# Performance work log

Hardware: AMD Instinct MI355X
Metric: run time of the kernel (lower is better)

The kernel has to match this reference:

```python
import jax, jax.numpy as jnp
import numpy as np

PROX_THRESH = 50.0
NEG_SLOPE = 0.2  # PyG GATConv default leaky_relu slope


def _layer_norm(x, g, b, eps=1e-5):
    m = x.mean(-1, keepdims=True)
    v = x.var(-1, keepdims=True)
    return (x - m) / jnp.sqrt(v + eps) * g + b


def _forward(ego_agent_past, neighbor_agents_past, node_w, node_b, node_ln_g,
             node_ln_b, ego_w, ego_b, ego_ln_g, ego_ln_b, gat_w, gat_asrc,
             gat_adst, gat_b, proj_w, proj_b):
    B = ego_agent_past.shape[0]
    ego_last = ego_agent_past[:, -1, :5]            # [B,5]
    nbr_last = neighbor_agents_past[:, :, -1, :5]   # [B,Nn,5]
    x = jnp.concatenate([ego_last[:, None], nbr_last], axis=1)  # [B,N,5]
    N = x.shape[1]
    dim = node_w.shape[1]
    heads, C = gat_asrc.shape[1], gat_asrc.shape[2]

    # build_graph: edge (j->i) iff dist(i,j) < 50 and i != j; GATConv then
    # adds self-loops, so the diagonal is always connected.
    pos = x[..., :2]
    d2 = jnp.sum((pos[:, :, None, :] - pos[:, None, :, :]) ** 2, axis=-1)  # [B,N,N]
    eye = jnp.eye(N, dtype=bool)
    adj = ((jnp.sqrt(d2) < PROX_THRESH) & ~eye) | eye   # adj[b,i,j]: msg j -> i

    # node features zero-padded from 5 -> 11 columns (as in forward)
    nf = jnp.pad(x, ((0, 0), (0, 0), (0, 11 - x.shape[-1])))
    h_node = _layer_norm(jax.nn.relu(nf @ node_w + node_b), node_ln_g, node_ln_b)
    h_ego = _layer_norm(jax.nn.relu(nf[..., :7] @ ego_w + ego_b), ego_ln_g, ego_ln_b)
    is_ego = (jnp.arange(N) == 0)  # node 0 of every scene is the ego
    h = jnp.where(is_ego[None, :, None], h_ego, h_node)  # [B,N,dim]

    # GATConv layers (eval mode, dropout inactive), concat=True
    for l in range(gat_w.shape[0]):
        wh = (h @ gat_w[l]).reshape(B, N, heads, C)                    # [B,N,H,C]
        a_s = jnp.einsum('bnhc,hc->bnh', wh, gat_asrc[l])              # source term
        a_d = jnp.einsum('bnhc,hc->bnh', wh, gat_adst[l])              # dest term
        # e[b,i,j,h] for edge j->i
        e = jax.nn.leaky_relu(a_s[:, None, :, :] + a_d[:, :, None, :], NEG_SLOPE)
        e = jnp.where(adj[..., None], e, -1e9)
        alpha = jax.nn.softmax(e, axis=2)                              # over sources j
        out = jnp.einsum('bijh,bjhc->bihc', alpha, wh).reshape(B, N, dim) + gat_b[l]
        h = jax.nn.relu(out)

    h = h @ proj_w + proj_b
    # all agents are valid (randn features have nonzero abs-sum), so no padding
    mask = jnp.zeros((B, N), dtype=bool)
    return h, mask


def setup_inputs() -> dict:
    key = jax.random.key(0)
    ks = jax.random.split(key, 10)
    B, Nn, T = 16, 1023, 20
    dim, heads, L = 256, 4, 2
    C = dim // heads
    f = lambda i, s: jax.random.normal(ks[i], s, dtype=jnp.float32)
    return {
        'ego_agent_past': f(0, (B, T, 7)),
        'neighbor_agents_past': f(1, (B, Nn, T, 11)),
        'node_w': f(2, (11, dim)) * 0.1, 'node_b': jnp.zeros((dim,), jnp.float32),
        'node_ln_g': jnp.ones((dim,), jnp.float32), 'node_ln_b': jnp.zeros((dim,), jnp.float32),
        'ego_w': f(3, (7, dim)) * 0.1, 'ego_b': jnp.zeros((dim,), jnp.float32),
        'ego_ln_g': jnp.ones((dim,), jnp.float32), 'ego_ln_b': jnp.zeros((dim,), jnp.float32),
        'gat_w': f(4, (L, dim, dim)) * 0.1,
        'gat_asrc': f(5, (L, heads, C)) * 0.1,
        'gat_adst': f(6, (L, heads, C)) * 0.1,
        'gat_b': jnp.zeros((L, dim), jnp.float32),
        'proj_w': f(7, (dim, dim)) * 0.1, 'proj_b': jnp.zeros((dim,), jnp.float32),
    }


def reference(ego_agent_past, neighbor_agents_past, node_w, node_b, node_ln_g,
              node_ln_b, ego_w, ego_b, ego_ln_g, ego_ln_b, gat_w, gat_asrc,
              gat_adst, gat_b, proj_w, proj_b):
    return _forward(ego_agent_past, neighbor_agents_past, node_w, node_b,
                    node_ln_g, node_ln_b, ego_w, ego_b, ego_ln_g, ego_ln_b,
                    gat_w, gat_asrc, gat_adst, gat_b, proj_w, proj_b)
```

## Files before the change

kernel.cpp:

```cpp
#include <hip/hip_runtime.h>
#include <cstddef>

typedef _Float16 f16;
typedef _Float16 f16x8 __attribute__((ext_vector_type(8)));
typedef _Float16 f16x4 __attribute__((ext_vector_type(4)));
typedef float f32x4 __attribute__((ext_vector_type(4)));

#define BATCH 16
#define NAGENT 1024
#define NNBR 1023
#define TSTEP 20
#define DIM 256
#define ROWS 16384
#define TH2 2500.0f
#define LOG2E 1.44269504089f

#define O_PX   0
#define O_PY   16384
#define O_H16  32768
#define O_AS   2129920
#define O_AD   2195456
#define O_M    2260992
#define O_US   2261056
#define O_UD   2263104
#define O_WT   2265152
#define O_ADJ  2363456

__global__ __launch_bounds__(256) void node_embed(
    const float* __restrict__ ego, const float* __restrict__ nbr,
    const float* __restrict__ node_w, const float* __restrict__ node_b,
    const float* __restrict__ node_g, const float* __restrict__ node_beta,
    const float* __restrict__ ego_w, const float* __restrict__ ego_b,
    const float* __restrict__ ego_g, const float* __restrict__ ego_beta,
    f16* __restrict__ h16, float* __restrict__ px, float* __restrict__ py) {
    int w = threadIdx.x >> 6, lane = threadIdx.x & 63;
    int row = blockIdx.x * 4 + w;
    int b = row >> 10, n = row & 1023;
    const float* src;
    if (n == 0) src = ego + (size_t)b * TSTEP * 7 + (TSTEP - 1) * 7;
    else        src = nbr + (((size_t)b * NNBR + (n - 1)) * TSTEP + (TSTEP - 1)) * 11;
    const float *W, *bias, *g, *beta;
    if (n == 0) { W = ego_w;  bias = ego_b;  g = ego_g;  beta = ego_beta; }
    else        { W = node_w; bias = node_b; g = node_g; beta = node_beta; }
    float xv[5];
#pragma unroll
    for (int k = 0; k < 5; k++) xv[k] = src[k];
    if (lane == 0) { px[row] = xv[0]; py[row] = xv[1]; }
    int c0 = lane * 4;
    float4 bv = *(const float4*)(bias + c0);
    float acc[4] = {bv.x, bv.y, bv.z, bv.w};
#pragma unroll
    for (int k = 0; k < 5; k++) {
        float4 wv = *(const float4*)(W + (size_t)k * 256 + c0);
        acc[0] = fmaf(xv[k], wv.x, acc[0]);
        acc[1] = fmaf(xv[k], wv.y, acc[1]);
        acc[2] = fmaf(xv[k], wv.z, acc[2]);
        acc[3] = fmaf(xv[k], wv.w, acc[3]);
    }
#pragma unroll
    for (int c = 0; c < 4; c++) acc[c] = fmaxf(acc[c], 0.f);
    float s1 = acc[0] + acc[1] + acc[2] + acc[3];
    float s2 = acc[0]*acc[0] + acc[1]*acc[1] + acc[2]*acc[2] + acc[3]*acc[3];
#pragma unroll
    for (int off = 1; off < 64; off <<= 1) {
        s1 += __shfl_xor(s1, off);
        s2 += __shfl_xor(s2, off);
    }
    float mean = s1 * (1.f / 256.f);
    float var  = s2 * (1.f / 256.f) - mean * mean;
    float rstd = rsqrtf(var + 1e-5f);
    float4 gv = *(const float4*)(g + c0);
    float4 be = *(const float4*)(beta + c0);
    f16x4 o;
    o[0] = (f16)((acc[0] - mean) * rstd * gv.x + be.x);
    o[1] = (f16)((acc[1] - mean) * rstd * gv.y + be.y);
    o[2] = (f16)((acc[2] - mean) * rstd * gv.z + be.z);
    o[3] = (f16)((acc[3] - mean) * rstd * gv.w + be.w);
    *(f16x4*)(h16 + (size_t)row * 256 + c0) = o;
}

__global__ __launch_bounds__(256) void adj_build(const float* __restrict__ px,
                                                 const float* __restrict__ py,
                                                 unsigned char* __restrict__ mask) {
    int blk = blockIdx.x;
    int b = blk >> 6, ic = blk & 63;
    int base = b << 10;
    __shared__ float sx[1024], sy[1024];
    int t = threadIdx.x;
#pragma unroll
    for (int i = 0; i < 4; i++) {
        sx[t + i * 256] = px[base + t + i * 256];
        sy[t + i * 256] = py[base + t + i * 256];
    }
    __syncthreads();
    int i_loc = t >> 4;
    int s = (t >> 3) & 1;
    int q = (t >> 1) & 3;
    int chalf = t & 1;
    int ig = ic * 16 + i_loc;
    float xi = sx[ig], yi = sy[ig];
    unsigned int w0 = 0, w1 = 0;
#pragma unroll
    for (int cc = 0; cc < 8; cc++) {
        int c = chalf * 8 + cc;
        unsigned int byte = 0;
        int j0 = s * 512 + c * 32 + q * 8;
#pragma unroll
        for (int jj = 0; jj < 8; jj++) {
            int j = j0 + jj;
            float dx = sx[j] - xi, dy = sy[j] - yi;
            if ((dx * dx + dy * dy < TH2) || (j == ig)) byte |= 1u << jj;
        }
        if (cc < 4) w0 |= byte << (cc * 8);
        else        w1 |= byte << ((cc - 4) * 8);
    }
    uint2 v; v.x = w0; v.y = w1;
    *(uint2*)(mask + (((size_t)(base + ig)) << 7) + s * 64 + q * 16 + chalf * 8) = v;
}

__global__ __launch_bounds__(256) void prep_weights(
    const float* __restrict__ gat_w, const float* __restrict__ proj_w,
    const float* __restrict__ asrc, const float* __restrict__ adst,
    f16* __restrict__ WT, float* __restrict__ us, float* __restrict__ ud) {
    int bid = blockIdx.x;
    int t = threadIdx.x;
    if (bid < 48) {
        int m = bid >> 4, t4 = bid & 15;
        int ti = (t4 >> 2) * 64;
        int tj = (t4 & 3) * 64;
        const float* W = (m < 2) ? (gat_w + (size_t)m * 65536) : proj_w;
        __shared__ float ls[64][68];
#pragma unroll
        for (int i = 0; i < 4; i++) {
            int idx = t + i * 256;
            int r = idx >> 4, c4 = (idx & 15) * 4;
            float4 v = *(const float4*)(W + (size_t)(ti + r) * 256 + tj + c4);
            ls[r][c4] = v.x; ls[r][c4 + 1] = v.y; ls[r][c4 + 2] = v.z; ls[r][c4 + 3] = v.w;
        }
        __syncthreads();
#pragma unroll
        for (int i = 0; i < 2; i++) {
            int idx = t + i * 256;
            int nr = idx >> 3, kc = (idx & 7) * 8;
            f16x8 v;
#pragma unroll
            for (int j = 0; j < 8; j++) v[j] = (f16)ls[kc + j][nr];
            *(f16x8*)(WT + (size_t)m * 65536 + (size_t)(tj + nr) * 256 + ti + kc) = v;
        }
    } else {
        int blk = bid - 48;
        int l = blk >> 2, h = blk & 3;
        const float* W  = gat_w + (size_t)l * 65536 + t * 256 + h * 64;
        const float* as = asrc + l * 256 + h * 64;
        const float* ad = adst + l * 256 + h * 64;
        float s = 0.f, d = 0.f;
#pragma unroll 8
        for (int c = 0; c < 64; c++) { s = fmaf(W[c], as[c], s); d = fmaf(W[c], ad[c], d); }
        us[blk * 256 + t] = s;
        ud[blk * 256 + t] = d;
    }
}

__global__ __launch_bounds__(256, 4) void gemm_f16(
    const f16* __restrict__ A, const f16* __restrict__ BT,
    f16* __restrict__ whT, float* __restrict__ outF, const float* __restrict__ bias,
    const float* __restrict__ us, const float* __restrict__ ud,
    float* __restrict__ a_sT, float* __restrict__ a_dT) {
    __shared__ f16 sA[32 * 264];
    __shared__ float sU[8 * 256];
    int t = threadIdx.x;
    int m0 = blockIdx.x * 32;
    {
        int r = t >> 3, u0 = (t & 7) * 4;
        const f16* gp = A + (size_t)(m0 + r) * 256 + u0 * 8;
        f16* lp = sA + r * 264 + u0 * 8;
#pragma unroll
        for (int u = 0; u < 4; u++)
            *(f16x8*)(lp + u * 8) = *(const f16x8*)(gp + u * 8);
    }
    if (us) {
#pragma unroll
        for (int i = 0; i < 4; i++) sU[t + i * 256] = us[t + i * 256];
#pragma unroll
        for (int i = 0; i < 4; i++) sU[1024 + t + i * 256] = ud[t + i * 256];
    }
    __syncthreads();
    int w = t >> 6, lane = t & 63, il = lane & 15, q = lane >> 4;
    int n0 = w * 64;
    f32x4 acc[2][4];
#pragma unroll
    for (int mt = 0; mt < 2; mt++)
#pragma unroll
        for (int nt = 0; nt < 4; nt++) acc[mt][nt] = (f32x4){0.f, 0.f, 0.f, 0.f};
    const f16* Bp  = BT + (size_t)(n0 + il) * 256 + q * 8;
    const f16* Ap0 = sA + il * 264 + q * 8;
#pragma unroll 2
    for (int ks = 0; ks < 256; ks += 32) {
        f16x8 a0 = *(const f16x8*)(Ap0 + ks);
        f16x8 a1 = *(const f16x8*)(Ap0 + 16 * 264 + ks);
        f16x8 b0 = *(const f16x8*)(Bp + ks);
        f16x8 b1 = *(const f16x8*)(Bp + 16 * 256 + ks);
        f16x8 b2 = *(const f16x8*)(Bp + 32 * 256 + ks);
        f16x8 b3 = *(const f16x8*)(Bp + 48 * 256 + ks);
        acc[0][0] = __builtin_amdgcn_mfma_f32_16x16x32_f16(a0, b0, acc[0][0], 0, 0, 0);
        acc[0][1] = __builtin_amdgcn_mfma_f32_16x16x32_f16(a0, b1, acc[0][1], 0, 0, 0);
        acc[0][2] = __builtin_amdgcn_mfma_f32_16x16x32_f16(a0, b2, acc[0][2], 0, 0, 0);
        acc[0][3] = __builtin_amdgcn_mfma_f32_16x16x32_f16(a0, b3, acc[0][3], 0, 0, 0);
        acc[1][0] = __builtin_amdgcn_mfma_f32_16x16x32_f16(a1, b0, acc[1][0], 0, 0, 0);
        acc[1][1] = __builtin_amdgcn_mfma_f32_16x16x32_f16(a1, b1, acc[1][1], 0, 0, 0);
        acc[1][2] = __builtin_amdgcn_mfma_f32_16x16x32_f16(a1, b2, acc[1][2], 0, 0, 0);
        acc[1][3] = __builtin_amdgcn_mfma_f32_16x16x32_f16(a1, b3, acc[1][3], 0, 0, 0);
    }
    if (whT) {
#pragma unroll
        for (int mt = 0; mt < 2; mt++)
#pragma unroll
            for (int nt = 0; nt < 4; nt++) {
                f16x4 v;
#pragma unroll
                for (int reg = 0; reg < 4; reg++) v[reg] = (f16)acc[mt][nt][reg];
                *(f16x4*)(whT + (size_t)(n0 + nt * 16 + il) * ROWS + m0 + mt * 16 + q * 4) = v;
            }
    } else {
#pragma unroll
        for (int nt = 0; nt < 4; nt++) {
            float bv = bias[n0 + nt * 16 + il];
#pragma unroll
            for (int mt = 0; mt < 2; mt++)
#pragma unroll
                for (int reg = 0; reg < 4; reg++)
                    outF[(size_t)(m0 + mt * 16 + q * 4 + reg) * 256 + n0 + nt * 16 + il] =
                        acc[mt][nt][reg] + bv;
        }
    }
    if (us) {
        int r2 = t >> 3, sub = t & 7;
        int hh = sub & 3, isD = sub >> 2;
        const float* uv = sU + isD * 1024 + hh * 256;
        const f16* ar = sA + r2 * 264;
        float d0 = 0.f;
#pragma unroll 4
        for (int kk = 0; kk < 32; kk++) {
            f16x8 av = *(const f16x8*)(ar + kk * 8);
            float4 u0 = *(const float4*)(uv + kk * 8);
            float4 u1 = *(const float4*)(uv + kk * 8 + 4);
            d0 += (float)av[0] * u0.x + (float)av[1] * u0.y +
                  (float)av[2] * u0.z + (float)av[3] * u0.w +
                  (float)av[4] * u1.x + (float)av[5] * u1.y +
                  (float)av[6] * u1.z + (float)av[7] * u1.w;
        }
        float* dst = isD ? a_dT : a_sT;
        dst[(size_t)hh * ROWS + m0 + r2] = d0;
    }
}

__global__ __launch_bounds__(256) void reduce_max(const float* __restrict__ a_sT,
                                                  float* __restrict__ M) {
    int blk = blockIdx.x;
    int b = blk >> 2, h = blk & 3;
    const float* p = a_sT + (size_t)h * ROWS + b * NAGENT;
    int t = threadIdx.x;
    float m = fmaxf(fmaxf(p[t], p[t + 256]), fmaxf(p[t + 512], p[t + 768]));
#pragma unroll
    for (int off = 32; off > 0; off >>= 1) m = fmaxf(m, __shfl_down(m, off));
    __shared__ float red[4];
    if ((t & 63) == 0) red[t >> 6] = m;
    __syncthreads();
    if (t == 0) M[blk] = fmaxf(fmaxf(red[0], red[1]), fmaxf(red[2], red[3]));
}

__global__ __launch_bounds__(512, 4) void gat_attn(
    const f16* __restrict__ whT, const float* __restrict__ a_sT,
    const float* __restrict__ a_dT, const unsigned char* __restrict__ mask,
    const float* __restrict__ M, const float* __restrict__ gat_b,
    f16* __restrict__ h16out) {
    __shared__ f32x4 comb[4][64][10];
    int t = threadIdx.x;
    int w = t >> 6, lane = t & 63;
    int h = w & 3, s = w >> 2;
    int blk = blockIdx.x;
    int b = blk >> 5;
    int i0 = (blk & 31) << 5;
    int base = b << 10;
    int il = lane & 15, q = lane >> 4;
    int ig0 = i0 + il, ig1 = i0 + 16 + il;

    float Mh = M[b * 4 + h];
    float adv0 = a_dT[(size_t)h * ROWS + base + ig0];
    float adv1 = a_dT[(size_t)h * ROWS + base + ig1];
    float mz0 = Mh + adv0, mz1 = Mh + adv1;
    float mi0 = fmaxf(mz0, 0.2f * mz0), mi1 = fmaxf(mz1, 0.2f * mz1);
    float nm0 = -mi0 * LOG2E, nm1 = -mi1 * LOG2E;

    uint4 mq0 = *(const uint4*)(mask + (((size_t)(base + ig0)) << 7) + s * 64 + q * 16);
    uint4 mq1 = *(const uint4*)(mask + (((size_t)(base + ig1)) << 7) + s * 64 + q * 16);
    unsigned int mw0[4] = {mq0.x, mq0.y, mq0.z, mq0.w};
    unsigned int mw1[4] = {mq1.x, mq1.y, mq1.z, mq1.w};

    f32x4 acc[2][5];
#pragma unroll
    for (int mt = 0; mt < 2; mt++)
#pragma unroll
        for (int nt = 0; nt < 5; nt++) acc[mt][nt] = (f32x4){0.f, 0.f, 0.f, 0.f};
    f16x8 ones;
#pragma unroll
    for (int j = 0; j < 8; j++) ones[j] = (f16)1.f;

    int jbase = base + (s << 9);
    const f16*   wp  = whT + (size_t)(h * 64 + il) * ROWS + jbase + q * 8;
    const float* asp = a_sT + (size_t)h * ROWS + jbase + q * 8;

    for (int c = 0; c < 16; ++c) {
        int j0 = c * 32;
        f16x8 b0 = *(const f16x8*)(wp + j0);
        f16x8 b1 = *(const f16x8*)(wp + (size_t)16 * ROWS + j0);
        f16x8 b2 = *(const f16x8*)(wp + (size_t)32 * ROWS + j0);
        f16x8 b3 = *(const f16x8*)(wp + (size_t)48 * ROWS + j0);
        float4 as0 = *(const float4*)(asp + j0);
        float4 as1 = *(const float4*)(asp + j0 + 4);
        unsigned int mb0 = (mw0[c >> 2] >> ((c & 3) * 8)) & 255u;
        unsigned int mb1 = (mw1[c >> 2] >> ((c & 3) * 8)) & 255u;
        float asv[8] = {as0.x, as0.y, as0.z, as0.w, as1.x, as1.y, as1.z, as1.w};
        f16x8 afr0, afr1;
#pragma unroll
        for (int jj = 0; jj < 8; ++jj) {
            float z = asv[jj];
            float z0 = z + adv0, z1 = z + adv1;
            float sc0 = fmaxf(z0, 0.2f * z0), sc1 = fmaxf(z1, 0.2f * z1);
            float e0 = exp2f(fmaf(sc0, LOG2E, nm0));
            float e1 = exp2f(fmaf(sc1, LOG2E, nm1));
            afr0[jj] = (f16)(((mb0 >> jj) & 1u) ? e0 : 0.f);
            afr1[jj] = (f16)(((mb1 >> jj) & 1u) ? e1 : 0.f);
        }
        acc[0][0] = __builtin_amdgcn_mfma_f32_16x16x32_f16(afr0, b0, acc[0][0], 0, 0, 0);
        acc[1][0] = __builtin_amdgcn_mfma_f32_16x16x32_f16(afr1, b0, acc[1][0], 0, 0, 0);
        acc[0][1] = __builtin_amdgcn_mfma_f32_16x16x32_f16(afr0, b1, acc[0][1], 0, 0, 0);
        acc[1][1] = __builtin_amdgcn_mfma_f32_16x16x32_f16(afr1, b1, acc[1][1], 0, 0, 0);
        acc[0][2] = __builtin_amdgcn_mfma_f32_16x16x32_f16(afr0, b2, acc[0][2], 0, 0, 0);
        acc[1][2] = __builtin_amdgcn_mfma_f32_16x16x32_f16(afr1, b2, acc[1][2], 0, 0, 0);
        acc[0][3] = __builtin_amdgcn_mfma_f32_16x16x32_f16(afr0, b3, acc[0][3], 0, 0, 0);
        acc[1][3] = __builtin_amdgcn_mfma_f32_16x16x32_f16(afr1, b3, acc[1][3], 0, 0, 0);
        acc[0][4] = __builtin_amdgcn_mfma_f32_16x16x32_f16(afr0, ones, acc[0][4], 0, 0, 0);
        acc[1][4] = __builtin_amdgcn_mfma_f32_16x16x32_f16(afr1, ones, acc[1][4], 0, 0, 0);
    }
    if (s == 1) {
#pragma unroll
        for (int mt = 0; mt < 2; mt++)
#pragma unroll
            for (int nt = 0; nt < 5; nt++) comb[h][lane][mt * 5 + nt] = acc[mt][nt];
    }
    __syncthreads();
    if (s == 0) {
#pragma unroll
        for (int mt = 0; mt < 2; mt++)
#pragma unroll
            for (int nt = 0; nt < 5; nt++) acc[mt][nt] += comb[h][lane][mt * 5 + nt];
        float b0v = gat_b[h * 64 + il];
        float b1v = gat_b[h * 64 + 16 + il];
        float b2v = gat_b[h * 64 + 32 + il];
        float b3v = gat_b[h * 64 + 48 + il];
#pragma unroll
        for (int mt = 0; mt < 2; mt++) {
#pragma unroll
            for (int reg = 0; reg < 4; ++reg) {
                float inv = 1.f / acc[mt][4][reg];
                size_t ro = (size_t)(base + i0 + mt * 16 + q * 4 + reg) * DIM + h * 64 + il;
                h16out[ro +  0] = (f16)fmaxf(fmaf(acc[mt][0][reg], inv, b0v), 0.f);
                h16out[ro + 16] = (f16)fmaxf(fmaf(acc[mt][1][reg], inv, b1v), 0.f);
                h16out[ro + 32] = (f16)fmaxf(fmaf(acc[mt][2][reg], inv, b2v), 0.f);
                h16out[ro + 48] = (f16)fmaxf(fmaf(acc[mt][3][reg], inv, b3v), 0.f);
            }
        }
    }
}

__global__ void zero_mask(float* __restrict__ p) {
    p[blockIdx.x * 256 + threadIdx.x] = 0.f;
}

extern "C" void kernel_launch(void* const* d_in, const int* in_sizes, int n_in,
                              void* d_out, int out_size, void* d_ws, size_t ws_size,
                              hipStream_t stream) {
    const float* ego       = (const float*)d_in[0];
    const float* nbr       = (const float*)d_in[1];
    const float* node_w    = (const float*)d_in[2];
    const float* node_b    = (const float*)d_in[3];
    const float* node_g    = (const float*)d_in[4];
    const float* node_beta = (const float*)d_in[5];
    const float* ego_w     = (const float*)d_in[6];
    const float* ego_b     = (const float*)d_in[7];
    const float* ego_g     = (const float*)d_in[8];
    const float* ego_beta  = (const float*)d_in[9];
    const float* gat_w     = (const float*)d_in[10];
    const float* gat_asrc  = (const float*)d_in[11];
    const float* gat_adst  = (const float*)d_in[12];
    const float* gat_bias  = (const float*)d_in[13];
    const float* proj_w    = (const float*)d_in[14];
    const float* proj_b    = (const float*)d_in[15];

    float* out = (float*)d_out;
    float* ws  = (float*)d_ws;
    float* px   = ws + O_PX;
    float* py   = ws + O_PY;
    f16*   h16  = (f16*)(ws + O_H16);
    float* asT  = ws + O_AS;
    float* adT  = ws + O_AD;
    float* Mmax = ws + O_M;
    float* us   = ws + O_US;
    float* ud   = ws + O_UD;
    f16*   WT   = (f16*)(ws + O_WT);
    unsigned char* adj = (unsigned char*)(ws + O_ADJ);
    f16*   whT  = (f16*)d_out;

    node_embed<<<4096, 256, 0, stream>>>(ego, nbr, node_w, node_b, node_g, node_beta,
                                         ego_w, ego_b, ego_g, ego_beta, h16, px, py);
    adj_build<<<1024, 256, 0, stream>>>(px, py, adj);
    prep_weights<<<56, 256, 0, stream>>>(gat_w, proj_w, gat_asrc, gat_adst, WT, us, ud);
    for (int l = 0; l < 2; l++) {
        gemm_f16<<<512, 256, 0, stream>>>(h16, WT + (size_t)l * 65536, whT, nullptr, nullptr,
                                          us + l * 1024, ud + l * 1024, asT, adT);
        reduce_max<<<64, 256, 0, stream>>>(asT, Mmax);
        gat_attn<<<512, 512, 0, stream>>>(whT, asT, adT, adj, Mmax,
                                          gat_bias + l * 256, h16);
    }
    gemm_f16<<<512, 256, 0, stream>>>(h16, WT + (size_t)2 * 65536, nullptr, out, proj_b,
                                      nullptr, nullptr, nullptr, nullptr);
    zero_mask<<<64, 256, 0, stream>>>(out + (size_t)ROWS * DIM);
}
```

Before: 252.4 us.

## Fuse prep kernels into one launch and fold source-max into GEMM via atomics

Merges node embedding, adjacency build, weight transpose, tail zeroing and Mmax init into a single mega_prep launch. The adjacency blocks now read positions straight from the inputs instead of an intermediate px/py buffer. The separate reduce_max kernel is removed: each GEMM block reduces its 32 a_s values per head and applies a CAS-based atomic max. The change also transposes the comb shared-memory layout in gat_attn and unrolls its main loop by two. The aim is fewer launches and less inter-kernel traffic, at the cost of atomic contention, an extra __syncthreads in the GEMM epilogue, and a heterogeneous grid.

Measured after the change: 259.9 us. +3.0%, slower.

```diff
diff --git a/kernel.cpp b/kernel.cpp
--- a/kernel.cpp
+++ b/kernel.cpp
@@ -14,150 +14,165 @@
 #define ROWS 16384
 #define TH2 2500.0f
 #define LOG2E 1.44269504089f
-
-#define O_PX   0
-#define O_PY   16384
-#define O_H16  32768
-#define O_AS   2129920
-#define O_AD   2195456
-#define O_M    2260992
-#define O_US   2261056
-#define O_UD   2263104
-#define O_WT   2265152
-#define O_ADJ  2363456
-
-__global__ __launch_bounds__(256) void node_embed(
+#define NEGBIG -3.0e38f
+
+#define O_H16  0
+#define O_AS   2097152
+#define O_AD   2162688
+#define O_US   2228224
+#define O_UD   2230272
+#define O_WT   2232320
+#define O_ADJ  2330624
+#define O_M    2854912
+
+__device__ inline void atomicMaxF(float* addr, float val) {
+    int* ai = (int*)addr;
+    int old = __float_as_int(*addr);
+    while (__int_as_float(old) < val) {
+        int assumed = old;
+        old = atomicCAS(ai, assumed, __float_as_int(val));
+        if (old == assumed) break;
+    }
+}
+
+__global__ __launch_bounds__(256) void mega_prep(
     const float* __restrict__ ego, const float* __restrict__ nbr,
     const float* __restrict__ node_w, const float* __restrict__ node_b,
     const float* __restrict__ node_g, const float* __restrict__ node_beta,
     const float* __restrict__ ego_w, const float* __restrict__ ego_b,
     const float* __restrict__ ego_g, const float* __restrict__ ego_beta,
-    f16* __restrict__ h16, float* __restrict__ px, float* __restrict__ py) {
-    int w = threadIdx.x >> 6, lane = threadIdx.x & 63;
-    int row = blockIdx.x * 4 + w;
-    int b = row >> 10, n = row & 1023;
-    const float* src;
-    if (n == 0) src = ego + (size_t)b * TSTEP * 7 + (TSTEP - 1) * 7;
-    else        src = nbr + (((size_t)b * NNBR + (n - 1)) * TSTEP + (TSTEP - 1)) * 11;
-    const float *W, *bias, *g, *beta;
-    if (n == 0) { W = ego_w;  bias = ego_b;  g = ego_g;  beta = ego_beta; }
-    else        { W = node_w; bias = node_b; g = node_g; beta = node_beta; }
-    float xv[5];
-#pragma unroll
-    for (int k = 0; k < 5; k++) xv[k] = src[k];
-    if (lane == 0) { px[row] = xv[0]; py[row] = xv[1]; }
-    int c0 = lane * 4;
-    float4 bv = *(const float4*)(bias + c0);
-    float acc[4] = {bv.x, bv.y, bv.z, bv.w};
-#pragma unroll
-    for (int k = 0; k < 5; k++) {
-        float4 wv = *(const float4*)(W + (size_t)k * 256 + c0);
-        acc[0] = fmaf(xv[k], wv.x, acc[0]);
-        acc[1] = fmaf(xv[k], wv.y, acc[1]);
-        acc[2] = fmaf(xv[k], wv.z, acc[2]);
-        acc[3] = fmaf(xv[k], wv.w, acc[3]);
-    }
-#pragma unroll
-    for (int c = 0; c < 4; c++) acc[c] = fmaxf(acc[c], 0.f);
-    float s1 = acc[0] + acc[1] + acc[2] + acc[3];
-    float s2 = acc[0]*acc[0] + acc[1]*acc[1] + acc[2]*acc[2] + acc[3]*acc[3];
-#pragma unroll
-    for (int off = 1; off < 64; off <<= 1) {
-        s1 += __shfl_xor(s1, off);
-        s2 += __shfl_xor(s2, off);
-    }
-    float mean = s1 * (1.f / 256.f);
-    float var  = s2 * (1.f / 256.f) - mean * mean;
-    float rstd = rsqrtf(var + 1e-5f);
-    float4 gv = *(const float4*)(g + c0);
-    float4 be = *(const float4*)(beta + c0);
-    f16x4 o;
-    o[0] = (f16)((acc[0] - mean) * rstd * gv.x + be.x);
-    o[1] = (f16)((acc[1] - mean) * rstd * gv.y + be.y);
-    o[2] = (f16)((acc[2] - mean) * rstd * gv.z + be.z);
-    o[3] = (f16)((acc[3] - mean) * rstd * gv.w + be.w);
-    *(f16x4*)(h16 + (size_t)row * 256 + c0) = o;
-}
-
-__global__ __launch_bounds__(256) void adj_build(const float* __restrict__ px,
-                                                 const float* __restrict__ py,
-                                                 unsigned char* __restrict__ mask) {
-    int blk = blockIdx.x;
-    int b = blk >> 6, ic = blk & 63;
-    int base = b << 10;
-    __shared__ float sx[1024], sy[1024];
-    int t = threadIdx.x;
-#pragma unroll
-    for (int i = 0; i < 4; i++) {
-        sx[t + i * 256] = px[base + t + i * 256];
-        sy[t + i * 256] = py[base + t + i * 256];
-    }
-    __syncthreads();
-    int i_loc = t >> 4;
-    int s = (t >> 3) & 1;
-    int q = (t >> 1) & 3;
-    int chalf = t & 1;
-    int ig = ic * 16 + i_loc;
-    float xi = sx[ig], yi = sy[ig];
-    unsigned int w0 = 0, w1 = 0;
-#pragma unroll
-    for (int cc = 0; cc < 8; cc++) {
-        int c = chalf * 8 + cc;
-        unsigned int byte = 0;
-        int j0 = s * 512 + c * 32 + q * 8;
-#pragma unroll
-        for (int jj = 0; jj < 8; jj++) {
-            int j = j0 + jj;
-            float dx = sx[j] - xi, dy = sy[j] - yi;
-            if ((dx * dx + dy * dy < TH2) || (j == ig)) byte |= 1u << jj;
-        }
-        if (cc < 4) w0 |= byte << (cc * 8);
-        else        w1 |= byte << ((cc - 4) * 8);
-    }
-    uint2 v; v.x = w0; v.y = w1;
-    *(uint2*)(mask + (((size_t)(base + ig)) << 7) + s * 64 + q * 16 + chalf * 8) = v;
-}
-
-__global__ __launch_bounds__(256) void prep_weights(
     const float* __restrict__ gat_w, const float* __restrict__ proj_w,
     const float* __restrict__ asrc, const float* __restrict__ adst,
-    f16* __restrict__ WT, float* __restrict__ us, float* __restrict__ ud) {
+    f16* __restrict__ h16, unsigned char* __restrict__ mask,
+    f16* __restrict__ WT, float* __restrict__ us, float* __restrict__ ud,
+    float* __restrict__ Mmax, float* __restrict__ outTail) {
+    __shared__ float smem[64 * 68];
     int bid = blockIdx.x;
     int t = threadIdx.x;
-    if (bid < 48) {
-        int m = bid >> 4, t4 = bid & 15;
-        int ti = (t4 >> 2) * 64;
-        int tj = (t4 & 3) * 64;
-        const float* W = (m < 2) ? (gat_w + (size_t)m * 65536) : proj_w;
-        __shared__ float ls[64][68];
+    if (bid < 4096) {
+        int w = t >> 6, lane = t & 63;
+        int row = bid * 4 + w;
+        int b = row >> 10, n = row & 1023;
+        const float* src;
+        if (n == 0) src = ego + (size_t)b * TSTEP * 7 + (TSTEP - 1) * 7;
+        else        src = nbr + (((size_t)b * NNBR + (n - 1)) * TSTEP + (TSTEP - 1)) * 11;
+        const float *W, *bias, *g, *beta;
+        if (n == 0) { W = ego_w;  bias = ego_b;  g = ego_g;  beta = ego_beta; }
+        else        { W = node_w; bias = node_b; g = node_g; beta = node_beta; }
+        float xv[5];
+#pragma unroll
+        for (int k = 0; k < 5; k++) xv[k] = src[k];
+        int c0 = lane * 4;
+        float4 bv = *(const float4*)(bias + c0);
+        float acc[4] = {bv.x, bv.y, bv.z, bv.w};
+#pragma unroll
+        for (int k = 0; k < 5; k++) {
+            float4 wv = *(const float4*)(W + (size_t)k * 256 + c0);
+            acc[0] = fmaf(xv[k], wv.x, acc[0]);
+            acc[1] = fmaf(xv[k], wv.y, acc[1]);
+            acc[2] = fmaf(xv[k], wv.z, acc[2]);
+            acc[3] = fmaf(xv[k], wv.w, acc[3]);
+        }
+#pragma unroll
+        for (int c = 0; c < 4; c++) acc[c] = fmaxf(acc[c], 0.f);
+        float s1 = acc[0] + acc[1] + acc[2] + acc[3];
+        float s2 = acc[0]*acc[0] + acc[1]*acc[1] + acc[2]*acc[2] + acc[3]*acc[3];
+#pragma unroll
+        for (int off = 1; off < 64; off <<= 1) {
+            s1 += __shfl_xor(s1, off);
+            s2 += __shfl_xor(s2, off);
+        }
+        float mean = s1 * (1.f / 256.f);
+        float var  = s2 * (1.f / 256.f) - mean * mean;
+        float rstd = rsqrtf(var + 1e-5f);
+        float4 gv = *(const float4*)(g + c0);
+        float4 be = *(const float4*)(beta + c0);
+        f16x4 o;
+        o[0] = (f16)((acc[0] - mean) * rstd * gv.x + be.x);
+        o[1] = (f16)((acc[1] - mean) * rstd * gv.y + be.y);
+        o[2] = (f16)((acc[2] - mean) * rstd * gv.z + be.z);
+        o[3] = (f16)((acc[3] - mean) * rstd * gv.w + be.w);
+        *(f16x4*)(h16 + (size_t)row * 256 + c0) = o;
+    } else if (bid < 5120) {
+        int bid2 = bid - 4096;
+        int b = bid2 >> 6, ic = bid2 & 63;
+        int base = b << 10;
+        float* sx = smem;
+        float* sy = smem + 1024;
 #pragma unroll
         for (int i = 0; i < 4; i++) {
-            int idx = t + i * 256;
-            int r = idx >> 4, c4 = (idx & 15) * 4;
-            float4 v = *(const float4*)(W + (size_t)(ti + r) * 256 + tj + c4);
-            ls[r][c4] = v.x; ls[r][c4 + 1] = v.y; ls[r][c4 + 2] = v.z; ls[r][c4 + 3] = v.w;
+            int r = t + i * 256;
+            const float* srcp = (r == 0)
+                ? (ego + (size_t)b * TSTEP * 7 + (TSTEP - 1) * 7)
+                : (nbr + (((size_t)b * NNBR + (r - 1)) * TSTEP + (TSTEP - 1)) * 11);
+            sx[r] = srcp[0];
+            sy[r] = srcp[1];
         }
         __syncthreads();
-#pragma unroll
-        for (int i = 0; i < 2; i++) {
-            int idx = t + i * 256;
-            int nr = idx >> 3, kc = (idx & 7) * 8;
-            f16x8 v;
-#pragma unroll
-            for (int j = 0; j < 8; j++) v[j] = (f16)ls[kc + j][nr];
-            *(f16x8*)(WT + (size_t)m * 65536 + (size_t)(tj + nr) * 256 + ti + kc) = v;
-        }
+        int i_loc = t >> 4;
+        int s = (t >> 3) & 1;
+        int q = (t >> 1) & 3;
+        int chalf = t & 1;
+        int ig = ic * 16 + i_loc;
+        float xi = sx[ig], yi = sy[ig];
+        unsigned int w0 = 0, w1 = 0;
+#pragma unroll
+        for (int cc = 0; cc < 8; cc++) {
+            int c = chalf * 8 + cc;
+            unsigned int byte = 0;
+            int j0 = s * 512 + c * 32 + q * 8;
+#pragma unroll
+            for (int jj = 0; jj < 8; jj++) {
+                int j = j0 + jj;
+                float dx = sx[j] - xi, dy = sy[j] - yi;
+                if ((dx * dx + dy * dy < TH2) || (j == ig)) byte |= 1u << jj;
+            }
+            if (cc < 4) w0 |= byte << (cc * 8);
+            else        w1 |= byte << ((cc - 4) * 8);
+        }
+        uint2 v; v.x = w0; v.y = w1;
+        *(uint2*)(mask + (((size_t)(base + ig)) << 7) + s * 64 + q * 16 + chalf * 8) = v;
+    } else if (bid < 5176) {
+        int bid3 = bid - 5120;
+        if (bid3 < 48) {
+            int m = bid3 >> 4, t4 = bid3 & 15;
+            int ti = (t4 >> 2) * 64;
+            int tj = (t4 & 3) * 64;
+            const float* W = (m < 2) ? (gat_w + (size_t)m * 65536) : proj_w;
+            float (*ls)[68] = (float(*)[68])smem;
+#pragma unroll
+            for (int i = 0; i < 4; i++) {
+                int idx = t + i * 256;
+                int r = idx >> 4, c4 = (idx & 15) * 4;
+                float4 v = *(const float4*)(W + (size_t)(ti + r) * 256 + tj + c4);
+                ls[r][c4] = v.x; ls[r][c4 + 1] = v.y; ls[r][c4 + 2] = v.z; ls[r][c4 + 3] = v.w;
+            }
+            __syncthreads();
+#pragma unroll
+            for (int i = 0; i < 2; i++) {
+                int idx = t + i * 256;
+                int nr = idx >> 3, kc = (idx & 7) * 8;
+                f16x8 v;
+#pragma unroll
+                for (int j = 0; j < 8; j++) v[j] = (f16)ls[kc + j][nr];
+                *(f16x8*)(WT + (size_t)m * 65536 + (size_t)(tj + nr) * 256 + ti + kc) = v;
+            }
+        } else {
+            int blk = bid3 - 48;
+            int l = blk >> 2, h = blk & 3;
+            const float* W  = gat_w + (size_t)l * 65536 + t * 256 + h * 64;
+            const float* as = asrc + l * 256 + h * 64;
+            const float* ad = adst + l * 256 + h * 64;
+            float s = 0.f, d = 0.f;
+#pragma unroll 8
+            for (int c = 0; c < 64; c++) { s = fmaf(W[c], as[c], s); d = fmaf(W[c], ad[c], d); }
+            us[blk * 256 + t] = s;
+            ud[blk * 256 + t] = d;
+        }
+    } else if (bid < 5240) {
+        outTail[(bid - 5176) * 256 + t] = 0.f;
     } else {
-        int blk = bid - 48;
-        int l = blk >> 2, h = blk & 3;
-        const float* W  = gat_w + (size_t)l * 65536 + t * 256 + h * 64;
-        const float* as = asrc + l * 256 + h * 64;
-        const float* ad = adst + l * 256 + h * 64;
-        float s = 0.f, d = 0.f;
-#pragma unroll 8
-        for (int c = 0; c < 64; c++) { s = fmaf(W[c], as[c], s); d = fmaf(W[c], ad[c], d); }
-        us[blk * 256 + t] = s;
-        ud[blk * 256 + t] = d;
+        if (t < 128) Mmax[t] = NEGBIG;
     }
 }
 
@@ -165,9 +180,10 @@
     const f16* __restrict__ A, const f16* __restrict__ BT,
     f16* __restrict__ whT, float* __restrict__ outF, const float* __restrict__ bias,
     const float* __restrict__ us, const float* __restrict__ ud,
-    float* __restrict__ a_sT, float* __restrict__ a_dT) {
+    float* __restrict__ a_sT, float* __restrict__ a_dT, float* __restrict__ Mmax) {
     __shared__ f16 sA[32 * 264];
     __shared__ float sU[8 * 256];
+    __shared__ float redmax[4][32];
     int t = threadIdx.x;
     int m0 = blockIdx.x * 32;
     {
@@ -251,22 +267,15 @@
         }
         float* dst = isD ? a_dT : a_sT;
         dst[(size_t)hh * ROWS + m0 + r2] = d0;
-    }
-}
-
-__global__ __launch_bounds__(256) void reduce_max(const float* __restrict__ a_sT,
-                                                  float* __restrict__ M) {
-    int blk = blockIdx.x;
-    int b = blk >> 2, h = blk & 3;
-    const float* p = a_sT + (size_t)h * ROWS + b * NAGENT;
-    int t = threadIdx.x;
-    float m = fmaxf(fmaxf(p[t], p[t + 256]), fmaxf(p[t + 512], p[t + 768]));
-#pragma unroll
-    for (int off = 32; off > 0; off >>= 1) m = fmaxf(m, __shfl_down(m, off));
-    __shared__ float red[4];
-    if ((t & 63) == 0) red[t >> 6] = m;
-    __syncthreads();
-    if (t == 0) M[blk] = fmaxf(fmaxf(red[0], red[1]), fmaxf(red[2], red[3]));
+        if (!isD) redmax[hh][r2] = d0;
+        __syncthreads();
+        if (t < 4) {
+            float m = redmax[t][0];
+#pragma unroll
+            for (int k = 1; k < 32; k++) m = fmaxf(m, redmax[t][k]);
+            atomicMaxF(&Mmax[(m0 >> 10) * 4 + t], m);
+        }
+    }
 }
 
 __global__ __launch_bounds__(512, 4) void gat_attn(
@@ -274,7 +283,7 @@
     const float* __restrict__ a_dT, const unsigned char* __restrict__ mask,
     const float* __restrict__ M, const float* __restrict__ gat_b,
     f16* __restrict__ h16out) {
-    __shared__ f32x4 comb[4][64][10];
+    __shared__ f32x4 comb[10][4][64];
     int t = threadIdx.x;
     int w = t >> 6, lane = t & 63;
     int h = w & 3, s = w >> 2;
@@ -310,6 +319,7 @@
     const f16*   wp  = whT + (size_t)(h * 64 + il) * ROWS + jbase + q * 8;
     const float* asp = a_sT + (size_t)h * ROWS + jbase + q * 8;
 
+#pragma unroll 2
     for (int c = 0; c < 16; ++c) {
         int j0 = c * 32;
         f16x8 b0 = *(const f16x8*)(wp + j0);
@@ -347,14 +357,14 @@
 #pragma unroll
         for (int mt = 0; mt < 2; mt++)
 #pragma unroll
-            for (int nt = 0; nt < 5; nt++) comb[h][lane][mt * 5 + nt] = acc[mt][nt];
+            for (int nt = 0; nt < 5; nt++) comb[mt * 5 + nt][h][lane] = acc[mt][nt];
     }
     __syncthreads();
     if (s == 0) {
 #pragma unroll
         for (int mt = 0; mt < 2; mt++)
 #pragma unroll
-            for (int nt = 0; nt < 5; nt++) acc[mt][nt] += comb[h][lane][mt * 5 + nt];
+            for (int nt = 0; nt < 5; nt++) acc[mt][nt] += comb[mt * 5 + nt][h][lane];
         float b0v = gat_b[h * 64 + il];
         float b1v = gat_b[h * 64 + 16 + il];
         float b2v = gat_b[h * 64 + 32 + il];
@@ -372,10 +382,6 @@
             }
         }
     }
-}
-
-__global__ void zero_mask(float* __restrict__ p) {
-    p[blockIdx.x * 256 + threadIdx.x] = 0.f;
 }
 
 extern "C" void kernel_launch(void* const* d_in, const int* in_sizes, int n_in,
@@ -400,30 +406,28 @@
 
     float* out = (float*)d_out;
     float* ws  = (float*)d_ws;
-    float* px   = ws + O_PX;
-    float* py   = ws + O_PY;
     f16*   h16  = (f16*)(ws + O_H16);
     float* asT  = ws + O_AS;
     float* adT  = ws + O_AD;
-    float* Mmax = ws + O_M;
     float* us   = ws + O_US;
     float* ud   = ws + O_UD;
     f16*   WT   = (f16*)(ws + O_WT);
     unsigned char* adj = (unsigned char*)(ws + O_ADJ);
+    float* Mmax = ws + O_M;
     f16*   whT  = (f16*)d_out;
 
-    node_embed<<<4096, 256, 0, stream>>>(ego, nbr, node_w, node_b, node_g, node_beta,
-                                         ego_w, ego_b, ego_g, ego_beta, h16, px, py);
-    adj_build<<<1024, 256, 0, stream>>>(px, py, adj);
-    prep_weights<<<56, 256, 0, stream>>>(gat_w, proj_w, gat_asrc, gat_adst, WT, us, ud);
+    mega_prep<<<5241, 256, 0, stream>>>(ego, nbr, node_w, node_b, node_g, node_beta,
+                                        ego_w, ego_b, ego_g, ego_beta,
+                                        gat_w, proj_w, gat_asrc, gat_adst,
+                                        h16, adj, WT, us, ud, Mmax,
+                                        out + (size_t)ROWS * DIM);
     for (int l = 0; l < 2; l++) {
         gemm_f16<<<512, 256, 0, stream>>>(h16, WT + (size_t)l * 65536, whT, nullptr, nullptr,
-                                          us + l * 1024, ud + l * 1024, asT, adT);
-        reduce_max<<<64, 256, 0, stream>>>(asT, Mmax);
-        gat_attn<<<512, 512, 0, stream>>>(whT, asT, adT, adj, Mmax,
+                                          us + l * 1024, ud + l * 1024, asT, adT,
+                                          Mmax + l * 64);
+        gat_attn<<<512, 512, 0, stream>>>(whT, asT, adT, adj, Mmax + l * 64,
                                           gat_bias + l * 256, h16);
     }
     gemm_f16<<<512, 256, 0, stream>>>(h16, WT + (size_t)2 * 65536, nullptr, out, proj_b,
-                                      nullptr, nullptr, nullptr, nullptr);
-    zero_mask<<<64, 256, 0, stream>>>(out + (size_t)ROWS * DIM);
+                                      nullptr, nullptr, nullptr, nullptr, nullptr);
 }
```

## Pre-swizzle GEMM weights into MFMA fragment order, pack f16 conversions, fix LDS layout

Applied to the files above, without the earlier changes.

prep_weights now writes the transposed weights directly in per-wave MFMA fragment order, so the GEMM reads B operands as contiguous 8-element chunks per lane instead of strided rows. The attention kernel converts pairs of exponentials with packed round-toward-zero conversions, which cuts per-element convert instructions. The combine buffer in LDS is reordered so lane is the innermost index, which avoids bank conflicts. Round-toward-zero conversion changes rounding slightly, and prep_weights now does uncoalesced strided global reads.

Result: faster. 239.7 us (-5.0%).

```diff
diff --git a/kernel.cpp b/kernel.cpp
--- a/kernel.cpp
+++ b/kernel.cpp
@@ -4,6 +4,7 @@
 typedef _Float16 f16;
 typedef _Float16 f16x8 __attribute__((ext_vector_type(8)));
 typedef _Float16 f16x4 __attribute__((ext_vector_type(4)));
+typedef __fp16 fp16x2 __attribute__((ext_vector_type(2)));
 typedef float f32x4 __attribute__((ext_vector_type(4)));
 
 #define BATCH 16
@@ -125,27 +126,21 @@
     int bid = blockIdx.x;
     int t = threadIdx.x;
     if (bid < 48) {
-        int m = bid >> 4, t4 = bid & 15;
-        int ti = (t4 >> 2) * 64;
-        int tj = (t4 & 3) * 64;
+        int m = bid >> 4, part = bid & 15;
         const float* W = (m < 2) ? (gat_w + (size_t)m * 65536) : proj_w;
-        __shared__ float ls[64][68];
-#pragma unroll
-        for (int i = 0; i < 4; i++) {
-            int idx = t + i * 256;
-            int r = idx >> 4, c4 = (idx & 15) * 4;
-            float4 v = *(const float4*)(W + (size_t)(ti + r) * 256 + tj + c4);
-            ls[r][c4] = v.x; ls[r][c4 + 1] = v.y; ls[r][c4 + 2] = v.z; ls[r][c4 + 3] = v.w;
-        }
-        __syncthreads();
+        f16* WO = WT + (size_t)m * 65536;
 #pragma unroll
         for (int i = 0; i < 2; i++) {
-            int idx = t + i * 256;
-            int nr = idx >> 3, kc = (idx & 7) * 8;
+            int chunk = part * 512 + i * 256 + t;
+            int lane = chunk & 63;
+            int ksnt = chunk >> 6;
+            int ks = ksnt & 7, nt = ksnt >> 3;
+            int n = nt * 16 + (lane & 15);
+            int k0 = ks * 32 + (lane >> 4) * 8;
             f16x8 v;
 #pragma unroll
-            for (int j = 0; j < 8; j++) v[j] = (f16)ls[kc + j][nr];
-            *(f16x8*)(WT + (size_t)m * 65536 + (size_t)(tj + nr) * 256 + ti + kc) = v;
+            for (int e = 0; e < 8; e++) v[e] = (f16)W[(size_t)(k0 + e) * 256 + n];
+            *(f16x8*)(WO + (size_t)chunk * 8) = v;
         }
     } else {
         int blk = bid - 48;
@@ -162,7 +157,7 @@
 }
 
 __global__ __launch_bounds__(256, 4) void gemm_f16(
-    const f16* __restrict__ A, const f16* __restrict__ BT,
+    const f16* __restrict__ A, const f16* __restrict__ BT2,
     f16* __restrict__ whT, float* __restrict__ outF, const float* __restrict__ bias,
     const float* __restrict__ us, const float* __restrict__ ud,
     float* __restrict__ a_sT, float* __restrict__ a_dT) {
@@ -192,16 +187,16 @@
     for (int mt = 0; mt < 2; mt++)
 #pragma unroll
         for (int nt = 0; nt < 4; nt++) acc[mt][nt] = (f32x4){0.f, 0.f, 0.f, 0.f};
-    const f16* Bp  = BT + (size_t)(n0 + il) * 256 + q * 8;
+    const f16* Bp  = BT2 + (size_t)w * 16384 + (size_t)lane * 8;
     const f16* Ap0 = sA + il * 264 + q * 8;
 #pragma unroll 2
-    for (int ks = 0; ks < 256; ks += 32) {
-        f16x8 a0 = *(const f16x8*)(Ap0 + ks);
-        f16x8 a1 = *(const f16x8*)(Ap0 + 16 * 264 + ks);
-        f16x8 b0 = *(const f16x8*)(Bp + ks);
-        f16x8 b1 = *(const f16x8*)(Bp + 16 * 256 + ks);
-        f16x8 b2 = *(const f16x8*)(Bp + 32 * 256 + ks);
-        f16x8 b3 = *(const f16x8*)(Bp + 48 * 256 + ks);
+    for (int ksi = 0; ksi < 8; ksi++) {
+        f16x8 a0 = *(const f16x8*)(Ap0 + ksi * 32);
+        f16x8 a1 = *(const f16x8*)(Ap0 + 16 * 264 + ksi * 32);
+        f16x8 b0 = *(const f16x8*)(Bp + ksi * 512);
+        f16x8 b1 = *(const f16x8*)(Bp + 4096 + ksi * 512);
+        f16x8 b2 = *(const f16x8*)(Bp + 8192 + ksi * 512);
+        f16x8 b3 = *(const f16x8*)(Bp + 12288 + ksi * 512);
         acc[0][0] = __builtin_amdgcn_mfma_f32_16x16x32_f16(a0, b0, acc[0][0], 0, 0, 0);
         acc[0][1] = __builtin_amdgcn_mfma_f32_16x16x32_f16(a0, b1, acc[0][1], 0, 0, 0);
         acc[0][2] = __builtin_amdgcn_mfma_f32_16x16x32_f16(a0, b2, acc[0][2], 0, 0, 0);
@@ -274,7 +269,7 @@
     const float* __restrict__ a_dT, const unsigned char* __restrict__ mask,
     const float* __restrict__ M, const float* __restrict__ gat_b,
     f16* __restrict__ h16out) {
-    __shared__ f32x4 comb[4][64][10];
+    __shared__ f32x4 comb[10][4][64];
     int t = threadIdx.x;
     int w = t >> 6, lane = t & 63;
     int h = w & 3, s = w >> 2;
@@ -321,17 +316,26 @@
         unsigned int mb0 = (mw0[c >> 2] >> ((c & 3) * 8)) & 255u;
         unsigned int mb1 = (mw1[c >> 2] >> ((c & 3) * 8)) & 255u;
         float asv[8] = {as0.x, as0.y, as0.z, as0.w, as1.x, as1.y, as1.z, as1.w};
-        f16x8 afr0, afr1;
-#pragma unroll
-        for (int jj = 0; jj < 8; ++jj) {
-            float z = asv[jj];
-            float z0 = z + adv0, z1 = z + adv1;
-            float sc0 = fmaxf(z0, 0.2f * z0), sc1 = fmaxf(z1, 0.2f * z1);
-            float e0 = exp2f(fmaf(sc0, LOG2E, nm0));
-            float e1 = exp2f(fmaf(sc1, LOG2E, nm1));
-            afr0[jj] = (f16)(((mb0 >> jj) & 1u) ? e0 : 0.f);
-            afr1[jj] = (f16)(((mb1 >> jj) & 1u) ? e1 : 0.f);
-        }
+        union { f16x8 v; fp16x2 hp[4]; } u0, u1;
+#pragma unroll
+        for (int jp = 0; jp < 4; ++jp) {
+            float va = asv[2 * jp], vb = asv[2 * jp + 1];
+            float za = va + adv0, zb = vb + adv0;
+            float zc = va + adv1, zd = vb + adv1;
+            float sa = fmaxf(za, 0.2f * za), sb = fmaxf(zb, 0.2f * zb);
+            float sc_ = fmaxf(zc, 0.2f * zc), sd = fmaxf(zd, 0.2f * zd);
+            float ea = exp2f(fmaf(sa, LOG2E, nm0));
+            float eb = exp2f(fmaf(sb, LOG2E, nm0));
+            float ec = exp2f(fmaf(sc_, LOG2E, nm1));
+            float ed = exp2f(fmaf(sd, LOG2E, nm1));
+            ea = ((mb0 >> (2 * jp)) & 1u) ? ea : 0.f;
+            eb = ((mb0 >> (2 * jp + 1)) & 1u) ? eb : 0.f;
+            ec = ((mb1 >> (2 * jp)) & 1u) ? ec : 0.f;
+            ed = ((mb1 >> (2 * jp + 1)) & 1u) ? ed : 0.f;
+            u0.hp[jp] = __builtin_amdgcn_cvt_pkrtz(ea, eb);
+            u1.hp[jp] = __builtin_amdgcn_cvt_pkrtz(ec, ed);
+        }
+        f16x8 afr0 = u0.v, afr1 = u1.v;
         acc[0][0] = __builtin_amdgcn_mfma_f32_16x16x32_f16(afr0, b0, acc[0][0], 0, 0, 0);
         acc[1][0] = __builtin_amdgcn_mfma_f32_16x16x32_f16(afr1, b0, acc[1][0], 0, 0, 0);
         acc[0][1] = __builtin_amdgcn_mfma_f32_16x16x32_f16(afr0, b1, acc[0][1], 0, 0, 0);
@@ -347,14 +351,14 @@
 #pragma unroll
         for (int mt = 0; mt < 2; mt++)
 #pragma unroll
-            for (int nt = 0; nt < 5; nt++) comb[h][lane][mt * 5 + nt] = acc[mt][nt];
+            for (int nt = 0; nt < 5; nt++) comb[mt * 5 + nt][h][lane] = acc[mt][nt];
     }
     __syncthreads();
     if (s == 0) {
 #pragma unroll
         for (int mt = 0; mt < 2; mt++)
 #pragma unroll
-            for (int nt = 0; nt < 5; nt++) acc[mt][nt] += comb[h][lane][mt * 5 + nt];
+            for (int nt = 0; nt < 5; nt++) acc[mt][nt] += comb[mt * 5 + nt][h][lane];
         float b0v = gat_b[h * 64 + il];
         float b1v = gat_b[h * 64 + 16 + il];
         float b2v = gat_b[h * 64 + 32 + il];
```
